# Optimization experiments

Measured on AMD Instinct MI355X. Metric: run time of the kernel, lower is better.

## Reference

```python
import jax, jax.numpy as jnp
import numpy as np

B = 1024   # batch
V = 256    # num variables
K = 64     # num categories per variable
M = 32     # input distribution nodes per variable
N0 = V * M # 8192 input nodes (global node ids 1..N0; id 0 reserved = 0.0)

# layer pair l: prod layer gathers F=2 children from previous sum/input node range,
# sum layer gathers C=32 element children with softmax-normalized params.
F = 2
C = 32
E_SIZES = [8192, 4096, 2048, 1024]   # elements per prod layer
S_SIZES = [4096, 2048, 1024, 1]      # sum nodes per sum layer (last = root)


def setup_inputs() -> dict:
    key = jax.random.key(0)
    ks = jax.random.split(key, 6)
    x = jax.random.randint(ks[0], (B, V), 0, K, dtype=jnp.int32)
    in_logits = jax.random.normal(ks[1], (N0, K), dtype=jnp.float32)
    w1 = jax.random.normal(ks[2], (S_SIZES[0], C), dtype=jnp.float32)
    w2 = jax.random.normal(ks[3], (S_SIZES[1], C), dtype=jnp.float32)
    w3 = jax.random.normal(ks[4], (S_SIZES[2], C), dtype=jnp.float32)
    w4 = jax.random.normal(ks[5], (S_SIZES[3], C), dtype=jnp.float32)
    rng = np.random.default_rng(0)
    # global node-id ranges of each layer's outputs (row 0 is the reserved node)
    # inputs: [1, 8193); S1: [8193, 12289); S2: [12289, 14337); S3: [14337, 15361)
    starts = [1, 1 + N0, 1 + N0 + S_SIZES[0], 1 + N0 + S_SIZES[0] + S_SIZES[1]]
    sizes = [N0] + S_SIZES[:3]
    pids, cids = [], []
    for l in range(4):
        pids.append(jnp.asarray(rng.integers(starts[l], starts[l] + sizes[l], (E_SIZES[l], F)), dtype=jnp.int32))
        # element ids 1..E_l (element 0 reserved = -inf, never referenced)
        cids.append(jnp.asarray(rng.integers(1, E_SIZES[l] + 1, (S_SIZES[l], C)), dtype=jnp.int32))
    return {
        'x': x, 'in_logits': in_logits,
        'w1': w1, 'w2': w2, 'w3': w3, 'w4': w4,
        'pids1': pids[0], 'pids2': pids[1], 'pids3': pids[2], 'pids4': pids[3],
        'cids1': cids[0], 'cids2': cids[1], 'cids3': cids[2], 'cids4': cids[3],
    }


def _forward(x, in_logits, ws, pids, cids):
    Bx = x.shape[0]
    x_t = x.T  # [V, B], matches inputs.permute(1, 0)
    vids = jnp.arange(N0) // M  # variable owning each input node
    # input layer: node_mars[i] = log_softmax(in_logits[i])[x[var(i)]]
    lp = jax.nn.log_softmax(in_logits, axis=1)             # [N0, K]
    inp = jnp.take_along_axis(lp, x_t[vids], axis=1)        # [N0, B]
    nm = jnp.concatenate([jnp.zeros((1, Bx), lp.dtype), inp], axis=0)  # node_mars, row0=0.0
    neg_inf = jnp.full((1, Bx), -jnp.inf, lp.dtype)         # element_mars row0 = -inf
    for p, c, w in zip(pids, cids, ws):
        # ProdLayer: element_mars = gather children log-mars and sum
        em = nm[p].sum(axis=1)                              # [E, B]
        em = jnp.concatenate([neg_inf, em], axis=0)         # [E+1, B]
        # SumLayer: logsumexp of child element mars + normalized log-params
        logw = jax.nn.log_softmax(w, axis=1)                # flat_softmax per sum node
        new = jax.nn.logsumexp(em[c] + logw[:, :, None], axis=1)  # [S, B]
        nm = jnp.concatenate([nm, new], axis=0)
    # root node lls, permuted back to [B, num_roots]
    return nm[-S_SIZES[-1]:].T


def reference(x, in_logits, w1, w2, w3, w4,
              pids1, pids2, pids3, pids4,
              cids1, cids2, cids3, cids4):
    return _forward(x, in_logits, (w1, w2, w3, w4),
                    (pids1, pids2, pids3, pids4),
                    (cids1, cids2, cids3, cids4))
```

## Files before the change

### kernel.cpp

```cpp
#include <hip/hip_runtime.h>
#include <math.h>

#define BB 1024
#define VV 256
#define KK 64
#define N0 8192
#define CC 32

#define LOG2E 1.4426950408889634f
#define LN2   0.6931471805599453f
#define W1SCALE 8192.0f
#define ROOT_LOG2_SCALE 104.0f

static __device__ __forceinline__ float flog2(float x) { return __builtin_amdgcn_logf(x); }
static __device__ __forceinline__ float bf2f(unsigned short u) {
    union { unsigned int i; float f; } c; c.i = (unsigned int)u << 16; return c.f;
}
static __device__ __forceinline__ unsigned short f2bf(float f) {
    union { float f; unsigned int i; } c; c.f = f;
    unsigned int r = c.i + 0x7FFFu + ((c.i >> 16) & 1u);
    return (unsigned short)(r >> 16);
}
static __device__ __forceinline__ float lo_f(unsigned int u) {
    union { unsigned int i; float f; } c; c.i = u << 16; return c.f;
}
static __device__ __forceinline__ float hi_f(unsigned int u) {
    union { unsigned int i; float f; } c; c.i = u & 0xFFFF0000u; return c.f;
}
static __device__ __forceinline__ unsigned int cvtpk(float a, float b) {
    unsigned int r;
    asm("v_cvt_pk_bf16_f32 %0, %1, %2" : "=v"(r) : "v"(a), "v"(b));
    return r;
}

__global__ void __launch_bounds__(256) k_prep(
        const float* __restrict__ logits,
        const float* __restrict__ w1, const float* __restrict__ w2,
        const float* __restrict__ w3, const float* __restrict__ w4,
        const int* __restrict__ cids1, const int* __restrict__ cids2,
        const int* __restrict__ cids3, const int* __restrict__ cids4,
        const int* __restrict__ pids1, const int* __restrict__ pids2,
        const int* __restrict__ pids3, const int* __restrict__ pids4,
        unsigned short* __restrict__ lpT, unsigned int* __restrict__ ppk,
        unsigned int* __restrict__ spk, ushort4* __restrict__ rpk) {
    int bid = blockIdx.x, tid = threadIdx.x;
    __shared__ unsigned short tile[16][64];
    if (bid < 512) {
        int k = tid & 63;
        int w = tid >> 6;
        #pragma unroll
        for (int r = 0; r < 4; ++r) {
            int row = w * 4 + r;
            int i = bid * 16 + row;
            float l = logits[(size_t)i * KK + k];
            float m = l;
            #pragma unroll
            for (int d = 32; d; d >>= 1) m = fmaxf(m, __shfl_xor(m, d));
            float e = __expf(l - m);
            float s = e;
            #pragma unroll
            for (int d = 32; d; d >>= 1) s += __shfl_xor(s, d);
            tile[row][k] = f2bf(e / s);
        }
        __syncthreads();
        if (tid < 128) {
            int kk = tid & 63, g = tid >> 6;
            uint4 o;
            o.x = (unsigned int)tile[g * 8 + 0][kk] | ((unsigned int)tile[g * 8 + 1][kk] << 16);
            o.y = (unsigned int)tile[g * 8 + 2][kk] | ((unsigned int)tile[g * 8 + 3][kk] << 16);
            o.z = (unsigned int)tile[g * 8 + 4][kk] | ((unsigned int)tile[g * 8 + 5][kk] << 16);
            o.w = (unsigned int)tile[g * 8 + 6][kk] | ((unsigned int)tile[g * 8 + 7][kk] << 16);
            *(uint4*)(lpT + (size_t)kk * N0 + bid * 16 + g * 8) = o;
        }
    } else if (bid < 960) {
        int group = tid >> 5;
        int lane = tid & 31;
        #pragma unroll
        for (int r = 0; r < 2; ++r) {
            int n = (bid - 512) * 16 + group * 2 + r;
            const float* wsrc; const int* csrc; float scale;
            if (n < 4096)      { wsrc = w1 + (size_t)n * CC;          csrc = cids1 + (size_t)n * CC;          scale = W1SCALE; }
            else if (n < 6144) { wsrc = w2 + (size_t)(n - 4096) * CC; csrc = cids2 + (size_t)(n - 4096) * CC; scale = 1.0f; }
            else               { wsrc = w3 + (size_t)(n - 6144) * CC; csrc = cids3 + (size_t)(n - 6144) * CC; scale = 1.0f; }
            float lw = wsrc[lane];
            float m = lw;
            #pragma unroll
            for (int d = 16; d; d >>= 1) m = fmaxf(m, __shfl_xor(m, d, 32));
            float e = __expf(lw - m);
            float s = e;
            #pragma unroll
            for (int d = 16; d; d >>= 1) s += __shfl_xor(s, d, 32);
            unsigned int cid8 = (unsigned int)(csrc[lane] - 1) * 8u;
            spk[(size_t)n * CC + lane] = cid8 | ((unsigned int)f2bf(e / s * scale) << 16);
        }
    } else if (bid < 974) {
        int b = bid - 960;
        #pragma unroll
        for (int j = 0; j < 4; ++j) {
            int idx = b * 1024 + j * 256 + tid;
            int p0, p1;
            if (idx < 8192)       { p0 = pids1[idx * 2] - 1;                p1 = pids1[idx * 2 + 1] - 1; }
            else if (idx < 12288) { int e = idx - 8192;  p0 = pids2[e * 2] - 8193;  p1 = pids2[e * 2 + 1] - 8193; }
            else                  { int e = idx - 12288; p0 = pids3[e * 2] - 12289; p1 = pids3[e * 2 + 1] - 12289; }
            ppk[idx] = ((unsigned int)p0 * 8u) | (((unsigned int)p1 * 8u) << 16);
        }
    } else {
        if (tid < CC) {
            float lw = w4[tid];
            float m = lw;
            #pragma unroll
            for (int d = 16; d; d >>= 1) m = fmaxf(m, __shfl_xor(m, d, 32));
            float e = __expf(lw - m);
            float s = e;
            #pragma unroll
            for (int d = 16; d; d >>= 1) s += __shfl_xor(s, d, 32);
            int el = cids4[tid] - 1;
            ushort4 r;
            r.x = (unsigned short)((pids4[el * 2]     - 14337) * 8);
            r.y = (unsigned short)((pids4[el * 2 + 1] - 14337) * 8);
            r.z = f2bf(e / s); r.w = 0;
            rpk[tid] = r;
        }
    }
}

template <typename NMP>
static __device__ __forceinline__ void do_layer(
        NMP nm4, uint2* em4,
        const unsigned int* __restrict__ pp, const unsigned int* __restrict__ sp,
        int E, int S, int tid, int nthr) {
    const char* nmB = (const char*)nm4;
    const char* emB = (const char*)em4;
    for (int e = tid; e < E; e += nthr * 4) {
        unsigned int pw[4];
        uint2 av[4], bv[4];
        int cnt = 0;
        #pragma unroll
        for (int j = 0; j < 4; ++j) {
            int ee = e + j * nthr;
            if (ee < E) { pw[j] = pp[ee]; ++cnt; }
        }
        #pragma unroll
        for (int j = 0; j < 4; ++j) {
            if (j < cnt) {
                av[j] = *(const uint2*)(nmB + (pw[j] & 0xFFFFu));
                bv[j] = *(const uint2*)(nmB + (pw[j] >> 16));
            }
        }
        #pragma unroll
        for (int j = 0; j < 4; ++j) {
            if (j < cnt) {
                uint2 o;
                o.x = cvtpk(lo_f(av[j].x) * lo_f(bv[j].x),
                            hi_f(av[j].x) * hi_f(bv[j].x));
                o.y = cvtpk(lo_f(av[j].y) * lo_f(bv[j].y),
                            hi_f(av[j].y) * hi_f(bv[j].y));
                em4[e + j * nthr] = o;
            }
        }
    }
    __syncthreads();
    for (int s = tid; s < S; s += nthr) {
        const uint4* base = (const uint4*)(sp + (size_t)s * CC);
        uint4 q[8];
        #pragma unroll
        for (int j = 0; j < 8; ++j) q[j] = base[j];
        unsigned int uu[32];
        #pragma unroll
        for (int j = 0; j < 8; ++j) {
            uu[j * 4 + 0] = q[j].x; uu[j * 4 + 1] = q[j].y;
            uu[j * 4 + 2] = q[j].z; uu[j * 4 + 3] = q[j].w;
        }
        float s0 = 0.f, s1 = 0.f, s2 = 0.f, s3 = 0.f;
        #pragma unroll
        for (int h = 0; h < 2; ++h) {
            uint2 t[16];
            #pragma unroll
            for (int c = 0; c < 16; ++c)
                t[c] = *(const uint2*)(emB + (uu[h * 16 + c] & 0xFFFFu));
            #pragma unroll
            for (int c = 0; c < 16; ++c) {
                float w = hi_f(uu[h * 16 + c]);
                s0 = fmaf(lo_f(t[c].x), w, s0);
                s1 = fmaf(hi_f(t[c].x), w, s1);
                s2 = fmaf(lo_f(t[c].y), w, s2);
                s3 = fmaf(hi_f(t[c].y), w, s3);
            }
        }
        uint2 o;
        o.x = cvtpk(s0, s1);
        o.y = cvtpk(s2, s3);
        nm4[s] = o;
    }
    __syncthreads();
}

template <typename NMP>
static __device__ __forceinline__ void do_root(NMP nm4, const ushort4* __restrict__ rpk,
                                               float* __restrict__ out, int b0, int tid) {
    const char* nmB = (const char*)nm4;
    if (tid < 128) {
        int col = tid >> 5, c = tid & 31;
        ushort4 r = rpk[c];
        int woff = (col >> 1) << 2;
        unsigned int wa = *(const unsigned int*)(nmB + r.x + woff);
        unsigned int wb = *(const unsigned int*)(nmB + r.y + woff);
        float va = (col & 1) ? hi_f(wa) : lo_f(wa);
        float vb = (col & 1) ? hi_f(wb) : lo_f(wb);
        float su = va * vb * bf2f(r.z);
        #pragma unroll
        for (int d = 16; d; d >>= 1) su += __shfl_xor(su, d);
        if (c == 0) out[b0 + col] = (flog2(su) - ROOT_LOG2_SCALE) * LN2;
    }
}

__global__ void __launch_bounds__(1024, 4) k_mega_lds(
        const int* __restrict__ x, const unsigned short* __restrict__ lpT,
        const unsigned int* __restrict__ ppk, const unsigned int* __restrict__ spk,
        const ushort4* __restrict__ rpk, float* __restrict__ out) {
    extern __shared__ uint2 smem2[];
    uint2* em4 = smem2;
    uint2* nm4 = smem2 + 8192;
    int* xv = (int*)(smem2 + 16384);
    int tid = threadIdx.x;
    int b0 = blockIdx.x * 4;

    {
        int c = tid >> 8, v = tid & 255;
        xv[tid] = x[(b0 + c) * VV + v];
    }
    __syncthreads();
    for (int i = tid; i < N0; i += 1024) {
        int v = i >> 5;
        unsigned int a = lpT[(size_t)xv[v]       * N0 + i];
        unsigned int b = lpT[(size_t)xv[256 + v] * N0 + i];
        unsigned int c = lpT[(size_t)xv[512 + v] * N0 + i];
        unsigned int d = lpT[(size_t)xv[768 + v] * N0 + i];
        uint2 o;
        o.x = a | (b << 16);
        o.y = c | (d << 16);
        nm4[i] = o;
    }
    __syncthreads();
    do_layer(nm4, em4, ppk,         spk,          8192, 4096, tid, 1024);
    do_layer(nm4, em4, ppk + 8192,  spk + 131072, 4096, 2048, tid, 1024);
    do_layer(nm4, em4, ppk + 12288, spk + 196608, 2048, 1024, tid, 1024);
    do_root(nm4, rpk, out, b0, tid);
}

__global__ void __launch_bounds__(1024, 4) k_mega_glb(
        const int* __restrict__ x, const unsigned short* __restrict__ lpT,
        const unsigned int* __restrict__ ppk, const unsigned int* __restrict__ spk,
        const ushort4* __restrict__ rpk, uint2* __restrict__ nmg,
        float* __restrict__ out) {
    extern __shared__ uint2 smem2[];
    uint2* em4 = smem2;
    uint2* nm4 = nmg + (size_t)blockIdx.x * 8192;
    int tid = threadIdx.x;
    int b0 = blockIdx.x * 4;

    for (int i = tid; i < N0; i += 1024) {
        int v = i >> 5;
        unsigned int a = lpT[(size_t)x[(b0 + 0) * VV + v] * N0 + i];
        unsigned int b = lpT[(size_t)x[(b0 + 1) * VV + v] * N0 + i];
        unsigned int c = lpT[(size_t)x[(b0 + 2) * VV + v] * N0 + i];
        unsigned int d = lpT[(size_t)x[(b0 + 3) * VV + v] * N0 + i];
        uint2 o;
        o.x = a | (b << 16);
        o.y = c | (d << 16);
        nm4[i] = o;
    }
    __syncthreads();
    do_layer(nm4, em4, ppk,         spk,          8192, 4096, tid, 1024);
    do_layer(nm4, em4, ppk + 8192,  spk + 131072, 4096, 2048, tid, 1024);
    do_layer(nm4, em4, ppk + 12288, spk + 196608, 2048, 1024, tid, 1024);
    do_root(nm4, rpk, out, b0, tid);
}

extern "C" void kernel_launch(void* const* d_in, const int* in_sizes, int n_in,
                              void* d_out, int out_size, void* d_ws, size_t ws_size,
                              hipStream_t stream) {
    const int*   x         = (const int*)  d_in[0];
    const float* in_logits = (const float*)d_in[1];
    const float* w1        = (const float*)d_in[2];
    const float* w2        = (const float*)d_in[3];
    const float* w3        = (const float*)d_in[4];
    const float* w4        = (const float*)d_in[5];
    const int*   pids1     = (const int*)  d_in[6];
    const int*   pids2     = (const int*)  d_in[7];
    const int*   pids3     = (const int*)  d_in[8];
    const int*   pids4     = (const int*)  d_in[9];
    const int*   cids1     = (const int*)  d_in[10];
    const int*   cids2     = (const int*)  d_in[11];
    const int*   cids3     = (const int*)  d_in[12];
    const int*   cids4     = (const int*)  d_in[13];
    float* out = (float*)d_out;

    char* ws = (char*)d_ws;
    unsigned short* lpT = (unsigned short*)ws;
    unsigned int*   ppk = (unsigned int*)(ws + 1048576);
    unsigned int*   spk = (unsigned int*)(ws + 1105920);
    ushort4*        rpk = (ushort4*)(ws + 2023424);
    uint2*          nmg = (uint2*)(ws + 2023936);

    k_prep<<<975, 256, 0, stream>>>(in_logits, w1, w2, w3, w4,
                                    cids1, cids2, cids3, cids4,
                                    pids1, pids2, pids3, pids4,
                                    lpT, ppk, spk, rpk);

    const int SMEM_A = 135168;
    const int SMEM_B = 65536;
    hipError_t e = hipFuncSetAttribute((const void*)k_mega_lds,
                                       hipFuncAttributeMaxDynamicSharedMemorySize, SMEM_A);
    if (e == hipSuccess) {
        k_mega_lds<<<256, 1024, SMEM_A, stream>>>(x, lpT, ppk, spk, rpk, out);
    } else {
        (void)hipGetLastError();
        hipFuncSetAttribute((const void*)k_mega_glb,
                            hipFuncAttributeMaxDynamicSharedMemorySize, SMEM_B);
        k_mega_glb<<<256, 1024, SMEM_B, stream>>>(x, lpT, ppk, spk, rpk, nmg, out);
    }
}
```

Measured before the change: 118.2 us.

## Process two batch columns per block instead of four, doubling grid size

Each block of the fused megakernel now handles 2 batch samples instead of 4, so node and element rows shrink from 8 to 4 bytes. The packed child offsets in the prep kernel are rescaled from ×8 to ×4 to match, LDS use halves, and the grid grows from 256 to 512 blocks. The aim is more blocks per CU and better latency hiding on the 256-CU GPU. The cost is that each block reloads the full structure and weight tables (ppk/spk) for half as many samples, which doubles that traffic and adds per-element index overhead.

```diff
diff --git a/kernel.cpp b/kernel.cpp
--- a/kernel.cpp
+++ b/kernel.cpp
@@ -90,8 +90,8 @@
             float s = e;
             #pragma unroll
             for (int d = 16; d; d >>= 1) s += __shfl_xor(s, d, 32);
-            unsigned int cid8 = (unsigned int)(csrc[lane] - 1) * 8u;
-            spk[(size_t)n * CC + lane] = cid8 | ((unsigned int)f2bf(e / s * scale) << 16);
+            unsigned int cid4 = (unsigned int)(csrc[lane] - 1) * 4u;
+            spk[(size_t)n * CC + lane] = cid4 | ((unsigned int)f2bf(e / s * scale) << 16);
         }
     } else if (bid < 974) {
         int b = bid - 960;
@@ -102,7 +102,7 @@
             if (idx < 8192)       { p0 = pids1[idx * 2] - 1;                p1 = pids1[idx * 2 + 1] - 1; }
             else if (idx < 12288) { int e = idx - 8192;  p0 = pids2[e * 2] - 8193;  p1 = pids2[e * 2 + 1] - 8193; }
             else                  { int e = idx - 12288; p0 = pids3[e * 2] - 12289; p1 = pids3[e * 2 + 1] - 12289; }
-            ppk[idx] = ((unsigned int)p0 * 8u) | (((unsigned int)p1 * 8u) << 16);
+            ppk[idx] = ((unsigned int)p0 * 4u) | (((unsigned int)p1 * 4u) << 16);
         }
     } else {
         if (tid < CC) {
@@ -116,8 +116,8 @@
             for (int d = 16; d; d >>= 1) s += __shfl_xor(s, d, 32);
             int el = cids4[tid] - 1;
             ushort4 r;
-            r.x = (unsigned short)((pids4[el * 2]     - 14337) * 8);
-            r.y = (unsigned short)((pids4[el * 2 + 1] - 14337) * 8);
+            r.x = (unsigned short)((pids4[el * 2]     - 14337) * 4);
+            r.y = (unsigned short)((pids4[el * 2 + 1] - 14337) * 4);
             r.z = f2bf(e / s); r.w = 0;
             rpk[tid] = r;
         }
@@ -126,14 +126,13 @@
 
 template <typename NMP>
 static __device__ __forceinline__ void do_layer(
-        NMP nm4, uint2* em4,
+        NMP nm4, unsigned int* em4,
         const unsigned int* __restrict__ pp, const unsigned int* __restrict__ sp,
         int E, int S, int tid, int nthr) {
     const char* nmB = (const char*)nm4;
     const char* emB = (const char*)em4;
     for (int e = tid; e < E; e += nthr * 4) {
-        unsigned int pw[4];
-        uint2 av[4], bv[4];
+        unsigned int pw[4], av[4], bv[4];
         int cnt = 0;
         #pragma unroll
         for (int j = 0; j < 4; ++j) {
@@ -143,19 +142,15 @@
         #pragma unroll
         for (int j = 0; j < 4; ++j) {
             if (j < cnt) {
-                av[j] = *(const uint2*)(nmB + (pw[j] & 0xFFFFu));
-                bv[j] = *(const uint2*)(nmB + (pw[j] >> 16));
+                av[j] = *(const unsigned int*)(nmB + (pw[j] & 0xFFFFu));
+                bv[j] = *(const unsigned int*)(nmB + (pw[j] >> 16));
             }
         }
         #pragma unroll
         for (int j = 0; j < 4; ++j) {
             if (j < cnt) {
-                uint2 o;
-                o.x = cvtpk(lo_f(av[j].x) * lo_f(bv[j].x),
-                            hi_f(av[j].x) * hi_f(bv[j].x));
-                o.y = cvtpk(lo_f(av[j].y) * lo_f(bv[j].y),
-                            hi_f(av[j].y) * hi_f(bv[j].y));
-                em4[e + j * nthr] = o;
+                em4[e + j * nthr] = cvtpk(lo_f(av[j]) * lo_f(bv[j]),
+                                          hi_f(av[j]) * hi_f(bv[j]));
             }
         }
     }
@@ -171,26 +166,21 @@
             uu[j * 4 + 0] = q[j].x; uu[j * 4 + 1] = q[j].y;
             uu[j * 4 + 2] = q[j].z; uu[j * 4 + 3] = q[j].w;
         }
-        float s0 = 0.f, s1 = 0.f, s2 = 0.f, s3 = 0.f;
-        #pragma unroll
-        for (int h = 0; h < 2; ++h) {
-            uint2 t[16];
-            #pragma unroll
-            for (int c = 0; c < 16; ++c)
-                t[c] = *(const uint2*)(emB + (uu[h * 16 + c] & 0xFFFFu));
-            #pragma unroll
-            for (int c = 0; c < 16; ++c) {
-                float w = hi_f(uu[h * 16 + c]);
-                s0 = fmaf(lo_f(t[c].x), w, s0);
-                s1 = fmaf(hi_f(t[c].x), w, s1);
-                s2 = fmaf(lo_f(t[c].y), w, s2);
-                s3 = fmaf(hi_f(t[c].y), w, s3);
+        float s0 = 0.f, s1 = 0.f;
+        #pragma unroll
+        for (int h = 0; h < 4; ++h) {
+            unsigned int t[8];
+            #pragma unroll
+            for (int c = 0; c < 8; ++c)
+                t[c] = *(const unsigned int*)(emB + (uu[h * 8 + c] & 0xFFFFu));
+            #pragma unroll
+            for (int c = 0; c < 8; ++c) {
+                float w = hi_f(uu[h * 8 + c]);
+                s0 = fmaf(lo_f(t[c]), w, s0);
+                s1 = fmaf(hi_f(t[c]), w, s1);
             }
         }
-        uint2 o;
-        o.x = cvtpk(s0, s1);
-        o.y = cvtpk(s2, s3);
-        nm4[s] = o;
+        nm4[s] = cvtpk(s0, s1);
     }
     __syncthreads();
 }
@@ -199,14 +189,13 @@
 static __device__ __forceinline__ void do_root(NMP nm4, const ushort4* __restrict__ rpk,
                                                float* __restrict__ out, int b0, int tid) {
     const char* nmB = (const char*)nm4;
-    if (tid < 128) {
+    if (tid < 64) {
         int col = tid >> 5, c = tid & 31;
         ushort4 r = rpk[c];
-        int woff = (col >> 1) << 2;
-        unsigned int wa = *(const unsigned int*)(nmB + r.x + woff);
-        unsigned int wb = *(const unsigned int*)(nmB + r.y + woff);
-        float va = (col & 1) ? hi_f(wa) : lo_f(wa);
-        float vb = (col & 1) ? hi_f(wb) : lo_f(wb);
+        unsigned int wa = *(const unsigned int*)(nmB + r.x);
+        unsigned int wb = *(const unsigned int*)(nmB + r.y);
+        float va = col ? hi_f(wa) : lo_f(wa);
+        float vb = col ? hi_f(wb) : lo_f(wb);
         float su = va * vb * bf2f(r.z);
         #pragma unroll
         for (int d = 16; d; d >>= 1) su += __shfl_xor(su, d);
@@ -214,18 +203,18 @@
     }
 }
 
-__global__ void __launch_bounds__(1024, 4) k_mega_lds(
+__global__ void __launch_bounds__(1024, 8) k_mega_lds(
         const int* __restrict__ x, const unsigned short* __restrict__ lpT,
         const unsigned int* __restrict__ ppk, const unsigned int* __restrict__ spk,
         const ushort4* __restrict__ rpk, float* __restrict__ out) {
-    extern __shared__ uint2 smem2[];
-    uint2* em4 = smem2;
-    uint2* nm4 = smem2 + 8192;
-    int* xv = (int*)(smem2 + 16384);
+    extern __shared__ unsigned int smem1[];
+    unsigned int* em4 = smem1;
+    unsigned int* nm4 = smem1 + 8192;
+    int* xv = (int*)(smem1 + 16384);
     int tid = threadIdx.x;
-    int b0 = blockIdx.x * 4;
-
-    {
+    int b0 = blockIdx.x * 2;
+
+    if (tid < 512) {
         int c = tid >> 8, v = tid & 255;
         xv[tid] = x[(b0 + c) * VV + v];
     }
@@ -234,12 +223,7 @@
         int v = i >> 5;
         unsigned int a = lpT[(size_t)xv[v]       * N0 + i];
         unsigned int b = lpT[(size_t)xv[256 + v] * N0 + i];
-        unsigned int c = lpT[(size_t)xv[512 + v] * N0 + i];
-        unsigned int d = lpT[(size_t)xv[768 + v] * N0 + i];
-        uint2 o;
-        o.x = a | (b << 16);
-        o.y = c | (d << 16);
-        nm4[i] = o;
+        nm4[i] = a | (b << 16);
     }
     __syncthreads();
     do_layer(nm4, em4, ppk,         spk,          8192, 4096, tid, 1024);
@@ -248,27 +232,22 @@
     do_root(nm4, rpk, out, b0, tid);
 }
 
-__global__ void __launch_bounds__(1024, 4) k_mega_glb(
+__global__ void __launch_bounds__(1024, 8) k_mega_glb(
         const int* __restrict__ x, const unsigned short* __restrict__ lpT,
         const unsigned int* __restrict__ ppk, const unsigned int* __restrict__ spk,
-        const ushort4* __restrict__ rpk, uint2* __restrict__ nmg,
+        const ushort4* __restrict__ rpk, unsigned int* __restrict__ nmg,
         float* __restrict__ out) {
-    extern __shared__ uint2 smem2[];
-    uint2* em4 = smem2;
-    uint2* nm4 = nmg + (size_t)blockIdx.x * 8192;
+    extern __shared__ unsigned int smem1[];
+    unsigned int* em4 = smem1;
+    unsigned int* nm4 = nmg + (size_t)blockIdx.x * 8192;
     int tid = threadIdx.x;
-    int b0 = blockIdx.x * 4;
+    int b0 = blockIdx.x * 2;
 
     for (int i = tid; i < N0; i += 1024) {
         int v = i >> 5;
         unsigned int a = lpT[(size_t)x[(b0 + 0) * VV + v] * N0 + i];
         unsigned int b = lpT[(size_t)x[(b0 + 1) * VV + v] * N0 + i];
-        unsigned int c = lpT[(size_t)x[(b0 + 2) * VV + v] * N0 + i];
-        unsigned int d = lpT[(size_t)x[(b0 + 3) * VV + v] * N0 + i];
-        uint2 o;
-        o.x = a | (b << 16);
-        o.y = c | (d << 16);
-        nm4[i] = o;
+        nm4[i] = a | (b << 16);
     }
     __syncthreads();
     do_layer(nm4, em4, ppk,         spk,          8192, 4096, tid, 1024);
@@ -301,23 +280,23 @@
     unsigned int*   ppk = (unsigned int*)(ws + 1048576);
     unsigned int*   spk = (unsigned int*)(ws + 1105920);
     ushort4*        rpk = (ushort4*)(ws + 2023424);
-    uint2*          nmg = (uint2*)(ws + 2023936);
+    unsigned int*   nmg = (unsigned int*)(ws + 2023936);
 
     k_prep<<<975, 256, 0, stream>>>(in_logits, w1, w2, w3, w4,
                                     cids1, cids2, cids3, cids4,
                                     pids1, pids2, pids3, pids4,
                                     lpT, ppk, spk, rpk);
 
-    const int SMEM_A = 135168;
-    const int SMEM_B = 65536;
+    const int SMEM_A = 67584;
+    const int SMEM_B = 32768;
     hipError_t e = hipFuncSetAttribute((const void*)k_mega_lds,
                                        hipFuncAttributeMaxDynamicSharedMemorySize, SMEM_A);
     if (e == hipSuccess) {
-        k_mega_lds<<<256, 1024, SMEM_A, stream>>>(x, lpT, ppk, spk, rpk, out);
+        k_mega_lds<<<512, 1024, SMEM_A, stream>>>(x, lpT, ppk, spk, rpk, out);
     } else {
         (void)hipGetLastError();
         hipFuncSetAttribute((const void*)k_mega_glb,
                             hipFuncAttributeMaxDynamicSharedMemorySize, SMEM_B);
-        k_mega_glb<<<256, 1024, SMEM_B, stream>>>(x, lpT, ppk, spk, rpk, nmg, out);
-    }
-}
+        k_mega_glb<<<512, 1024, SMEM_B, stream>>>(x, lpT, ppk, spk, rpk, nmg, out);
+    }
+}
```

Measured after the change: 144.7 us. 22.4% more time.
